# Kernel optimization log

Measured on AMD Instinct MI355X. Metric: run time of the kernel, lower is better.

Reference implementation:

```python
import jax, jax.numpy as jnp
import numpy as np

N_VARS = 4096      # number of discrete variables
CARD = 16          # uniform cardinality per variable
N_HIDDEN = 256
POP = 1024         # pop_size (batch)
N_VISIBLE = N_VARS * CARD  # 65536


def setup_inputs() -> dict:
    key = jax.random.key(0)
    k1, k2, k3 = jax.random.split(key, 3)
    # hidden units are binary stochastic in the RBM; uniform [0,1) works for the math
    hidden = jax.random.uniform(k1, (POP, N_HIDDEN), dtype=jnp.float32)
    W = jax.random.normal(k2, (N_VISIBLE, N_HIDDEN), dtype=jnp.float32) * 0.01
    a = jax.random.normal(k3, (N_VISIBLE,), dtype=jnp.float32) * 0.01
    return {"hidden": hidden, "W": W, "a": a}


def reference(hidden, W, a):
    # prob_visible_given_hidden: activation = hidden @ W^T + a  -> [POP, N_VISIBLE]
    act = jnp.einsum('bh,vh->bv', hidden, W) + a
    # per-variable segmented softmax over each block of CARD visible units
    # (uniform cardinality -> reshape to [POP, N_VARS, CARD] and softmax on last axis)
    prob = jax.nn.softmax(act.reshape(POP, N_VARS, CARD), axis=-1)
    return prob.reshape(POP, N_VISIBLE)
```

## Files before the change

kernel.cpp:

```cpp
#include <hip/hip_runtime.h>


typedef short  bf16x8 __attribute__((ext_vector_type(8)));
typedef float  f32x4  __attribute__((ext_vector_type(4)));

#define NH    256
#define POP   1024
#define NVIS  65536
#define BN    128
#define MBLK  256

__device__ __forceinline__ unsigned pack2bf(float lo, float hi) {
  return (__float_as_uint(hi) & 0xffff0000u) | (__float_as_uint(lo) >> 16);
}

__global__ __launch_bounds__(256, 2) void rbm_fused_kernel(
    const float* __restrict__ Hg,
    const float* __restrict__ Wg,
    const float* __restrict__ Ag,
    float* __restrict__ out)
{
  __shared__ short sB[8 * BN * 32];

  const int tid  = threadIdx.x;
  const int lane = tid & 63;
  const int wave = tid >> 6;
  const int quad = lane >> 4;
  const int col  = lane & 15;
  const int n_base = blockIdx.x * BN;
  const int m0     = blockIdx.y * MBLK + wave * 64;

  {
    const int row  = tid >> 1;
    const int half = (tid & 1) * 16;
    const float* src = Hg + (size_t)(n_base + row) * NH + half;
    #pragma unroll
    for (int j = 0; j < 8; ++j) {
      const float4 f0 = ((const float4*)(src + j * 32))[0];
      const float4 f1 = ((const float4*)(src + j * 32))[1];
      const float4 f2 = ((const float4*)(src + j * 32))[2];
      const float4 f3 = ((const float4*)(src + j * 32))[3];
      uint4 u0, u1;
      u0.x = pack2bf(f0.x, f0.y); u0.y = pack2bf(f0.z, f0.w);
      u0.z = pack2bf(f1.x, f1.y); u0.w = pack2bf(f1.z, f1.w);
      u1.x = pack2bf(f2.x, f2.y); u1.y = pack2bf(f2.z, f2.w);
      u1.z = pack2bf(f3.x, f3.y); u1.w = pack2bf(f3.z, f3.w);
      *(uint4*)&sB[(j * BN + row) * 32 + half]     = u0;
      *(uint4*)&sB[(j * BN + row) * 32 + half + 8] = u1;
    }
  }
  __syncthreads();

  f32x4 acc[4][8];
  #pragma unroll
  for (int mt = 0; mt < 4; ++mt)
    #pragma unroll
    for (int nt = 0; nt < 8; ++nt)
      acc[mt][nt] = f32x4{0.f, 0.f, 0.f, 0.f};

  const float* ap[4];
  #pragma unroll
  for (int mt = 0; mt < 4; ++mt)
    ap[mt] = Wg + (size_t)(m0 + mt * 16 + col) * NH + quad * 8;

  float4 pf[4][2];
  #pragma unroll
  for (int mt = 0; mt < 4; ++mt) {
    pf[mt][0] = ((const float4*)ap[mt])[0];
    pf[mt][1] = ((const float4*)ap[mt])[1];
  }

  #pragma unroll
  for (int j = 0; j < 8; ++j) {
    bf16x8 af[4];
    #pragma unroll
    for (int mt = 0; mt < 4; ++mt) {
      union { bf16x8 v; uint4 u; } cv;
      cv.u.x = pack2bf(pf[mt][0].x, pf[mt][0].y);
      cv.u.y = pack2bf(pf[mt][0].z, pf[mt][0].w);
      cv.u.z = pack2bf(pf[mt][1].x, pf[mt][1].y);
      cv.u.w = pack2bf(pf[mt][1].z, pf[mt][1].w);
      af[mt] = cv.v;
    }
    if (j < 7) {
      #pragma unroll
      for (int mt = 0; mt < 4; ++mt) {
        const float4* p = (const float4*)(ap[mt] + (j + 1) * 32);
        pf[mt][0] = p[0];
        pf[mt][1] = p[1];
      }
    }
    const short* bbase = &sB[(j * BN) * 32 + quad * 8];
    #pragma unroll
    for (int nt = 0; nt < 8; ++nt) {
      const bf16x8 bf = *(const bf16x8*)(bbase + (nt * 16 + col) * 32);
      #pragma unroll
      for (int mt = 0; mt < 4; ++mt)
        acc[mt][nt] = __builtin_amdgcn_mfma_f32_16x16x32_bf16(
            af[mt], bf, acc[mt][nt], 0, 0, 0);
    }
  }

  #pragma unroll
  for (int mt = 0; mt < 4; ++mt) {
    const int v0 = m0 + mt * 16 + quad * 4;
    const float4 av = *(const float4*)(Ag + v0);
    #pragma unroll
    for (int nt = 0; nt < 8; ++nt) {
      f32x4 c = acc[mt][nt];
      float x0 = c[0] + av.x, x1 = c[1] + av.y;
      float x2 = c[2] + av.z, x3 = c[3] + av.w;
      float mx = fmaxf(fmaxf(x0, x1), fmaxf(x2, x3));
      mx = fmaxf(mx, __shfl_xor(mx, 16));
      mx = fmaxf(mx, __shfl_xor(mx, 32));
      float e0 = __expf(x0 - mx), e1 = __expf(x1 - mx);
      float e2 = __expf(x2 - mx), e3 = __expf(x3 - mx);
      float s = (e0 + e1) + (e2 + e3);
      s += __shfl_xor(s, 16);
      s += __shfl_xor(s, 32);
      const float inv = 1.0f / s;
      f32x4 o;
      o[0] = e0 * inv; o[1] = e1 * inv; o[2] = e2 * inv; o[3] = e3 * inv;
      acc[mt][nt] = o;
    }
  }

  #pragma unroll
  for (int mt = 0; mt < 4; ++mt) {
    const int v0 = m0 + mt * 16 + quad * 4;
    #pragma unroll
    for (int nt = 0; nt < 8; ++nt) {
      const int b = n_base + nt * 16 + col;
      __builtin_nontemporal_store(acc[mt][nt],
                                  (f32x4*)(out + (size_t)b * NVIS + v0));
    }
  }
}

extern "C" void kernel_launch(void* const* d_in, const int* in_sizes, int n_in,
                              void* d_out, int out_size, void* d_ws, size_t ws_size,
                              hipStream_t stream) {
  const float* hidden = (const float*)d_in[0];
  const float* W      = (const float*)d_in[1];
  const float* a      = (const float*)d_in[2];
  float* out          = (float*)d_out;
  (void)d_ws; (void)ws_size;

  dim3 grid(POP / BN, NVIS / MBLK);
  rbm_fused_kernel<<<grid, 256, 0, stream>>>(hidden, W, a, out);
}
```

Baseline: 408.8 us.

## Halve batch tile, swizzle blocks across XCDs, relayout LDS for contiguous fragment reads

Shrinks the per-block batch tile from 128 to 64 rows, which cuts accumulator registers and lets occupancy rise to 3 blocks per CU. Uses a 1D grid whose block index is remapped so that the 16 batch panels sharing the same W slice land on the same XCD, to improve L2 reuse of W. Rearranges the hidden tile in LDS so each lane reads its bf16x8 fragment contiguously, avoiding bank conflicts. The cost is that each W slice is now loaded and converted by twice as many blocks.

```diff
diff --git a/kernel.cpp b/kernel.cpp
--- a/kernel.cpp
+++ b/kernel.cpp
@@ -7,67 +7,68 @@
 #define NH    256
 #define POP   1024
 #define NVIS  65536
-#define BN    128
+#define BN    64
 #define MBLK  256
+#define NT    4
 
 __device__ __forceinline__ unsigned pack2bf(float lo, float hi) {
   return (__float_as_uint(hi) & 0xffff0000u) | (__float_as_uint(lo) >> 16);
 }
 
-__global__ __launch_bounds__(256, 2) void rbm_fused_kernel(
+__global__ __launch_bounds__(256, 3) void rbm_fused_kernel(
     const float* __restrict__ Hg,
     const float* __restrict__ Wg,
     const float* __restrict__ Ag,
     float* __restrict__ out)
 {
-  __shared__ short sB[8 * BN * 32];
+  __shared__ short sB[8 * NT * 64 * 8];
 
   const int tid  = threadIdx.x;
   const int lane = tid & 63;
   const int wave = tid >> 6;
   const int quad = lane >> 4;
   const int col  = lane & 15;
-  const int n_base = blockIdx.x * BN;
-  const int m0     = blockIdx.y * MBLK + wave * 64;
+
+  const int id    = blockIdx.x;
+  const int xcd   = id & 7;
+  const int qq    = id >> 3;
+  const int mblk  = xcd + 8 * (qq >> 4);
+  const int panel = qq & 15;
+  const int n_base = panel * BN;
+  const int m0     = mblk * MBLK + wave * 64;
 
   {
-    const int row  = tid >> 1;
-    const int half = (tid & 1) * 16;
-    const float* src = Hg + (size_t)(n_base + row) * NH + half;
+    const int r   = tid >> 2;
+    const int sub = tid & 3;
+    const float* src = Hg + (size_t)(n_base + r) * NH + sub * 8;
+    short* dst = &sB[((r >> 4) * 64 + sub * 16 + (r & 15)) * 8];
     #pragma unroll
     for (int j = 0; j < 8; ++j) {
       const float4 f0 = ((const float4*)(src + j * 32))[0];
       const float4 f1 = ((const float4*)(src + j * 32))[1];
-      const float4 f2 = ((const float4*)(src + j * 32))[2];
-      const float4 f3 = ((const float4*)(src + j * 32))[3];
-      uint4 u0, u1;
-      u0.x = pack2bf(f0.x, f0.y); u0.y = pack2bf(f0.z, f0.w);
-      u0.z = pack2bf(f1.x, f1.y); u0.w = pack2bf(f1.z, f1.w);
-      u1.x = pack2bf(f2.x, f2.y); u1.y = pack2bf(f2.z, f2.w);
-      u1.z = pack2bf(f3.x, f3.y); u1.w = pack2bf(f3.z, f3.w);
-      *(uint4*)&sB[(j * BN + row) * 32 + half]     = u0;
-      *(uint4*)&sB[(j * BN + row) * 32 + half + 8] = u1;
+      uint4 u;
+      u.x = pack2bf(f0.x, f0.y); u.y = pack2bf(f0.z, f0.w);
+      u.z = pack2bf(f1.x, f1.y); u.w = pack2bf(f1.z, f1.w);
+      *(uint4*)(dst + j * (NT * 64 * 8)) = u;
     }
   }
   __syncthreads();
 
-  f32x4 acc[4][8];
+  f32x4 acc[4][NT];
   #pragma unroll
   for (int mt = 0; mt < 4; ++mt)
     #pragma unroll
-    for (int nt = 0; nt < 8; ++nt)
+    for (int nt = 0; nt < NT; ++nt)
       acc[mt][nt] = f32x4{0.f, 0.f, 0.f, 0.f};
 
-  const float* ap[4];
-  #pragma unroll
-  for (int mt = 0; mt < 4; ++mt)
-    ap[mt] = Wg + (size_t)(m0 + mt * 16 + col) * NH + quad * 8;
+  const float* abase = Wg + (size_t)(m0 + col) * NH + quad * 8;
 
   float4 pf[4][2];
   #pragma unroll
   for (int mt = 0; mt < 4; ++mt) {
-    pf[mt][0] = ((const float4*)ap[mt])[0];
-    pf[mt][1] = ((const float4*)ap[mt])[1];
+    const float4* p = (const float4*)(abase + (size_t)mt * 16 * NH);
+    pf[mt][0] = p[0];
+    pf[mt][1] = p[1];
   }
 
   #pragma unroll
@@ -85,15 +86,16 @@
     if (j < 7) {
       #pragma unroll
       for (int mt = 0; mt < 4; ++mt) {
-        const float4* p = (const float4*)(ap[mt] + (j + 1) * 32);
+        const float4* p =
+            (const float4*)(abase + (size_t)mt * 16 * NH + (j + 1) * 32);
         pf[mt][0] = p[0];
         pf[mt][1] = p[1];
       }
     }
-    const short* bbase = &sB[(j * BN) * 32 + quad * 8];
+    const short* bb = &sB[j * (NT * 64 * 8) + lane * 8];
     #pragma unroll
-    for (int nt = 0; nt < 8; ++nt) {
-      const bf16x8 bf = *(const bf16x8*)(bbase + (nt * 16 + col) * 32);
+    for (int nt = 0; nt < NT; ++nt) {
+      const bf16x8 bf = *(const bf16x8*)(bb + nt * (64 * 8));
       #pragma unroll
       for (int mt = 0; mt < 4; ++mt)
         acc[mt][nt] = __builtin_amdgcn_mfma_f32_16x16x32_bf16(
@@ -106,7 +108,7 @@
     const int v0 = m0 + mt * 16 + quad * 4;
     const float4 av = *(const float4*)(Ag + v0);
     #pragma unroll
-    for (int nt = 0; nt < 8; ++nt) {
+    for (int nt = 0; nt < NT; ++nt) {
       f32x4 c = acc[mt][nt];
       float x0 = c[0] + av.x, x1 = c[1] + av.y;
       float x2 = c[2] + av.z, x3 = c[3] + av.w;
@@ -129,7 +131,7 @@
   for (int mt = 0; mt < 4; ++mt) {
     const int v0 = m0 + mt * 16 + quad * 4;
     #pragma unroll
-    for (int nt = 0; nt < 8; ++nt) {
+    for (int nt = 0; nt < NT; ++nt) {
       const int b = n_base + nt * 16 + col;
       __builtin_nontemporal_store(acc[mt][nt],
                                   (f32x4*)(out + (size_t)b * NVIS + v0));
@@ -146,6 +148,6 @@
   float* out          = (float*)d_out;
   (void)d_ws; (void)ws_size;
 
-  dim3 grid(POP / BN, NVIS / MBLK);
-  rbm_fused_kernel<<<grid, 256, 0, stream>>>(hidden, W, a, out);
+  const int nblocks = (POP / BN) * (NVIS / MBLK);
+  rbm_fused_kernel<<<nblocks, 256, 0, stream>>>(hidden, W, a, out);
 }
```

Result: slower. 471.6 us (+15.4%).
